# Kernel tuning notes

Hardware: AMD Instinct MI355X
Metric: run time of the kernel (lower is better)

Reference implementation:

```python
import jax, jax.numpy as jnp
import numpy as np

N = 512          # num_satellites
STATE_DIM = 6    # pos(3) + vel(3)
OBJ_DIM = 58
F = STATE_DIM + OBJ_DIM          # node feature dim = 64
HID = (128, 64, 32)
EDGE_IN = 2 * F + 1              # sender + receiver + distance
NODE_IN = F + HID[-1]            # node feats + aggregated messages


def _linear_init(key, d_in, d_out):
    kw, _ = jax.random.split(key)
    w = jax.random.normal(kw, (d_in, d_out), jnp.float32) / np.sqrt(d_in).astype(np.float32)
    b = jnp.zeros((d_out,), jnp.float32)
    return w, b


def setup_inputs() -> dict:
    key = jax.random.key(0)
    ks = jax.random.split(key, 12)
    ew0, eb0 = _linear_init(ks[0], EDGE_IN, HID[0])
    ew1, eb1 = _linear_init(ks[1], HID[0], HID[1])
    ew2, eb2 = _linear_init(ks[2], HID[1], HID[2])
    nw0, nb0 = _linear_init(ks[3], NODE_IN, HID[0])
    nw1, nb1 = _linear_init(ks[4], HID[0], HID[1])
    nw2, nb2 = _linear_init(ks[5], HID[1], HID[2])
    nwo, nbo = _linear_init(ks[6], HID[2], F)   # residual projection back to F
    rw, rb = _linear_init(ks[7], F, 3)          # control readout
    states = jax.random.normal(ks[8], (N, STATE_DIM), jnp.float32)
    objectives = jax.random.normal(ks[9], (OBJ_DIM,), jnp.float32)
    return dict(states=states, objectives=objectives,
                ew0=ew0, eb0=eb0, ew1=ew1, eb1=eb1, ew2=ew2, eb2=eb2,
                nw0=nw0, nb0=nb0, nw1=nw1, nb1=nb1, nw2=nw2, nb2=nb2,
                nwo=nwo, nbo=nbo, rw=rw, rb=rb,
                num_message_passing=3)


def _edge_index(n):
    ii, jj = np.meshgrid(np.arange(n), np.arange(n), indexing='ij')
    m = ii != jj
    return jnp.asarray(ii[m]), jnp.asarray(jj[m])  # sender i, receiver j; E = n*(n-1)


def reference(states, objectives, ew0, eb0, ew1, eb1, ew2, eb2,
              nw0, nb0, nw1, nb1, nw2, nb2, nwo, nbo, rw, rb,
              num_message_passing):
    n = states.shape[0]
    snd, rcv = _edge_index(n)
    # node features: state concat broadcast objectives -> [N, F]
    nf = jnp.concatenate(
        [states, jnp.broadcast_to(objectives, (n, objectives.shape[0]))], axis=-1)
    # distances from raw states (constant across iterations): [E, 1]
    rel = states[rcv, :3] - states[snd, :3]
    dist = jnp.linalg.norm(rel, axis=-1, keepdims=True)
    relu = jax.nn.relu
    for _ in range(num_message_passing):
        # edge MLP over all E edges: [E, 2F+1] -> [E, 32]
        x = jnp.concatenate([nf[snd], nf[rcv], dist], axis=-1)
        h = relu(x @ ew0 + eb0)
        h = relu(h @ ew1 + eb1)
        msg = relu(h @ ew2 + eb2)
        # sum-aggregate incoming messages at receiver j: [N, 32]
        agg = jax.ops.segment_sum(msg, rcv, num_segments=n)
        # node MLP + residual: [N, F+32] -> [N, F]
        y = jnp.concatenate([nf, agg], axis=-1)
        h = relu(y @ nw0 + nb0)
        h = relu(h @ nw1 + nb1)
        h = relu(h @ nw2 + nb2)
        nf = nf + h @ nwo + nbo
    # control readout: [N, 3]
    return nf @ rw + rb
```

## Files before the change

### kernel.cpp

```cpp
#include <hip/hip_runtime.h>
#include <math.h>

#define NSAT 512
#define FDIM 64
#define H0D  128
#define H1D  64
#define H2D  32
#define NGRP 8
#define SB   64

#define KP1 68

#define WS_NF    0
#define WS_PRES  (WS_NF   + NSAT * FDIM)
#define WS_PRER  (WS_PRES + NSAT * H0D)
#define WS_AGG   (WS_PRER + NSAT * H0D)
#define WS_WT    (WS_AGG  + NGRP * NSAT * H2D)

using short8_t = __attribute__((ext_vector_type(8))) short;
using short4_t = __attribute__((ext_vector_type(4))) short;
using floatx4  = __attribute__((ext_vector_type(4))) float;
using floatx16 = __attribute__((ext_vector_type(16))) float;

__device__ __forceinline__ void split_ru(float x, short& hi, short& lo) {
    unsigned u = __builtin_bit_cast(unsigned, x);
    unsigned hb = (u + 0x8000u) >> 16;
    hi = (short)hb;
    float r = x - __builtin_bit_cast(float, hb << 16);
    lo = (short)((__builtin_bit_cast(unsigned, r) + 0x8000u) >> 16);
}

__global__ void prep_weights_kernel(const float* __restrict__ ew1,
                                    const float* __restrict__ ew2,
                                    short* __restrict__ w1A_hi,
                                    short* __restrict__ w1A_lo,
                                    short* __restrict__ w2t_hi,
                                    short* __restrict__ w2t_lo) {
    int e = blockIdx.x * 256 + threadIdx.x;
    if (e < H1D * H0D) {
        int j  = e & 7;
        int l  = (e >> 3) & 63;
        int kk = (e >> 9) & 7;
        int mh = e >> 12;
        int m = mh * 32 + (l & 31);
        int k = (l >> 5) * 64 + kk * 8 + j;
        short hi, lo; split_ru(ew1[k * H1D + m], hi, lo);
        w1A_hi[e] = hi; w1A_lo[e] = lo;
    } else if (e < H1D * H0D + H2D * H1D) {
        int e2 = e - H1D * H0D;
        int c = e2 >> 6, k = e2 & 63;
        short hi, lo; split_ru(ew2[k * H2D + c], hi, lo);
        w2t_hi[e2] = hi; w2t_lo[e2] = lo;
    }
}

__device__ __forceinline__ void compute_pre(const float* __restrict__ nfl,
                                            const float* __restrict__ ew0,
                                            const float* __restrict__ eb0,
                                            int i, int t,
                                            float* __restrict__ preSA,
                                            float* __restrict__ preR) {
    if (t < H0D) {
        int k = t;
        float s0 = 0.f, s1 = 0.f, s2 = 0.f, s3 = 0.f;
        #pragma unroll
        for (int f = 0; f < FDIM; f += 4) {
            s0 = fmaf(nfl[f + 0], ew0[(f + 0) * H0D + k], s0);
            s1 = fmaf(nfl[f + 1], ew0[(f + 1) * H0D + k], s1);
            s2 = fmaf(nfl[f + 2], ew0[(f + 2) * H0D + k], s2);
            s3 = fmaf(nfl[f + 3], ew0[(f + 3) * H0D + k], s3);
        }
        int kk = (k >> 3) & 7, lhi = k >> 6, j = k & 7;
        preSA[((i >> 5) * 8 + kk) * 512 + (lhi * 32 + (i & 31)) * 8 + j] =
            (s0 + s1) + (s2 + s3);
    } else {
        int k = t - H0D;
        float s0 = eb0[k], s1 = 0.f, s2 = 0.f, s3 = 0.f;
        #pragma unroll
        for (int f = 0; f < FDIM; f += 4) {
            s0 = fmaf(nfl[f + 0], ew0[(FDIM + f + 0) * H0D + k], s0);
            s1 = fmaf(nfl[f + 1], ew0[(FDIM + f + 1) * H0D + k], s1);
            s2 = fmaf(nfl[f + 2], ew0[(FDIM + f + 2) * H0D + k], s2);
            s3 = fmaf(nfl[f + 3], ew0[(FDIM + f + 3) * H0D + k], s3);
        }
        preR[i * H0D + k] = (s0 + s1) + (s2 + s3);
    }
}

__global__ void init_node_kernel(const float* __restrict__ states,
                                 const float* __restrict__ objectives,
                                 const float* __restrict__ ew0,
                                 const float* __restrict__ eb0,
                                 float* __restrict__ nf,
                                 float* __restrict__ preSA,
                                 float* __restrict__ preR) {
    __shared__ float nfl[FDIM];
    int i = blockIdx.x, t = threadIdx.x;
    if (t < FDIM) {
        float v = (t < 6) ? states[i * 6 + t] : objectives[t - 6];
        nfl[t] = v;
        nf[i * FDIM + t] = v;
    }
    __syncthreads();
    compute_pre(nfl, ew0, eb0, i, t, preSA, preR);
}

__global__ __launch_bounds__(256, 4)
void edge_agg_kernel(const float* __restrict__ states,
                     const float* __restrict__ preSA,
                     const float* __restrict__ preR,
                     const float* __restrict__ ew0,
                     const float* __restrict__ eb1,
                     const float* __restrict__ eb2,
                     const short* __restrict__ w1A_hi,
                     const short* __restrict__ w1A_lo,
                     const short* __restrict__ w2t_hi,
                     const short* __restrict__ w2t_lo,
                     float* __restrict__ aggP) {
    __shared__ __align__(16) short h1_hi[SB * KP1];
    __shared__ __align__(16) short h1_lo[SB * KP1];
    __shared__ __align__(16) float preR_l[H0D];
    __shared__ __align__(16) float wd_l[H0D];
    __shared__ float d_l[SB];
    __shared__ __align__(16) float eb1_l[H1D];
    __shared__ float eb2_l[H2D];
    __shared__ __align__(16) float red_l[4 * H2D];

    int t = threadIdx.x, b = blockIdx.x;
    int j = b >> 3, g = b & 7;
    int w = t >> 6, lane = t & 63;
    int mhalf = w >> 1, shalf = w & 1;
    int lhi = lane >> 5, llo = lane & 31;

    if (t < H0D) preR_l[t] = preR[j * H0D + t];
    else         wd_l[t - H0D] = ew0[H0D * H0D + (t - H0D)];
    if (t < SB) {
        int s = g * SB + t;
        float dx = states[s * 6 + 0] - states[j * 6 + 0];
        float dy = states[s * 6 + 1] - states[j * 6 + 1];
        float dz = states[s * 6 + 2] - states[j * 6 + 2];
        d_l[t] = sqrtf(dx * dx + dy * dy + dz * dz);
    } else if (t < 128) {
        eb1_l[t - 64] = eb1[t - 64];
    } else if (t < 160) {
        eb2_l[t - 128] = eb2[t - 128];
    }
    __syncthreads();

    int G = g * 2 + shalf;
    float d = d_l[shalf * 32 + llo];
    const float* pS = preSA + (G * 8) * 512 + lane * 8;
    const short* pAh = w1A_hi + mhalf * 4096 + lane * 8;
    const short* pAl = w1A_lo + mhalf * 4096 + lane * 8;

    floatx16 acc1;
    #pragma unroll
    for (int r = 0; r < 16; ++r) acc1[r] = 0.f;

    #pragma unroll
    for (int kk = 0; kk < 8; ++kk) {
        float4 a0 = *(const float4*)(pS + kk * 512);
        float4 a1 = *(const float4*)(pS + kk * 512 + 4);
        int kb = lhi * 64 + kk * 8;
        float4 r0 = *(const float4*)&preR_l[kb];
        float4 r1 = *(const float4*)&preR_l[kb + 4];
        float4 q0 = *(const float4*)&wd_l[kb];
        float4 q1 = *(const float4*)&wd_l[kb + 4];
        float v[8];
        v[0] = fmaxf(a0.x + fmaf(d, q0.x, r0.x), 0.f);
        v[1] = fmaxf(a0.y + fmaf(d, q0.y, r0.y), 0.f);
        v[2] = fmaxf(a0.z + fmaf(d, q0.z, r0.z), 0.f);
        v[3] = fmaxf(a0.w + fmaf(d, q0.w, r0.w), 0.f);
        v[4] = fmaxf(a1.x + fmaf(d, q1.x, r1.x), 0.f);
        v[5] = fmaxf(a1.y + fmaf(d, q1.y, r1.y), 0.f);
        v[6] = fmaxf(a1.z + fmaf(d, q1.z, r1.z), 0.f);
        v[7] = fmaxf(a1.w + fmaf(d, q1.w, r1.w), 0.f);
        short8_t bh, bl;
        #pragma unroll
        for (int e = 0; e < 8; ++e) {
            short hi, lo; split_ru(v[e], hi, lo);
            bh[e] = hi; bl[e] = lo;
        }
        short8_t ah = *(const short8_t*)(pAh + kk * 512);
        short8_t al = *(const short8_t*)(pAl + kk * 512);
        acc1 = __builtin_amdgcn_mfma_f32_32x32x16_bf16(ah, bh, acc1, 0, 0, 0);
        acc1 = __builtin_amdgcn_mfma_f32_32x32x16_bf16(ah, bl, acc1, 0, 0, 0);
        acc1 = __builtin_amdgcn_mfma_f32_32x32x16_bf16(al, bh, acc1, 0, 0, 0);
    }

    {
        int s1 = shalf * 32 + llo;
        #pragma unroll
        for (int q = 0; q < 4; ++q) {
            int m0 = mhalf * 32 + q * 8 + lhi * 4;
            short4_t ph, pl; short hi, lo;
            #pragma unroll
            for (int r = 0; r < 4; ++r) {
                float v = fmaxf(acc1[q * 4 + r] + eb1_l[m0 + r], 0.f);
                split_ru(v, hi, lo);
                ph[r] = hi; pl[r] = lo;
            }
            *(short4_t*)&h1_hi[s1 * KP1 + m0] = ph;
            *(short4_t*)&h1_lo[s1 * KP1 + m0] = pl;
        }
    }
    __syncthreads();

    int lq = lane >> 4, l15 = lane & 15;
    int s2loc = w * 16 + l15;
    floatx4 acc2a, acc2b;
    #pragma unroll
    for (int r = 0; r < 4; ++r) { acc2a[r] = 0.f; acc2b[r] = 0.f; }
    int bo2 = s2loc * KP1 + lq * 8;
    const short* pA2h0 = w2t_hi + l15 * H1D + lq * 8;
    const short* pA2l0 = w2t_lo + l15 * H1D + lq * 8;
    const short* pA2h1 = w2t_hi + (16 + l15) * H1D + lq * 8;
    const short* pA2l1 = w2t_lo + (16 + l15) * H1D + lq * 8;
    #pragma unroll
    for (int kk = 0; kk < 2; ++kk) {
        short4_t b0 = *(const short4_t*)&h1_hi[bo2 + kk * 32];
        short4_t b1 = *(const short4_t*)&h1_hi[bo2 + kk * 32 + 4];
        short4_t c0 = *(const short4_t*)&h1_lo[bo2 + kk * 32];
        short4_t c1 = *(const short4_t*)&h1_lo[bo2 + kk * 32 + 4];
        short8_t bh = __builtin_shufflevector(b0, b1, 0, 1, 2, 3, 4, 5, 6, 7);
        short8_t bl = __builtin_shufflevector(c0, c1, 0, 1, 2, 3, 4, 5, 6, 7);
        short8_t a0h = *(const short8_t*)(pA2h0 + kk * 32);
        short8_t a0l = *(const short8_t*)(pA2l0 + kk * 32);
        short8_t a1h = *(const short8_t*)(pA2h1 + kk * 32);
        short8_t a1l = *(const short8_t*)(pA2l1 + kk * 32);
        acc2a = __builtin_amdgcn_mfma_f32_16x16x32_bf16(a0h, bh, acc2a, 0, 0, 0);
        acc2a = __builtin_amdgcn_mfma_f32_16x16x32_bf16(a0h, bl, acc2a, 0, 0, 0);
        acc2a = __builtin_amdgcn_mfma_f32_16x16x32_bf16(a0l, bh, acc2a, 0, 0, 0);
        acc2b = __builtin_amdgcn_mfma_f32_16x16x32_bf16(a1h, bh, acc2b, 0, 0, 0);
        acc2b = __builtin_amdgcn_mfma_f32_16x16x32_bf16(a1h, bl, acc2b, 0, 0, 0);
        acc2b = __builtin_amdgcn_mfma_f32_16x16x32_bf16(a1l, bh, acc2b, 0, 0, 0);
    }

    {
        int sg = g * SB + s2loc;
        bool self = (sg == j);
        float red[8];
        #pragma unroll
        for (int r = 0; r < 4; ++r) {
            float v = fmaxf(acc2a[r] + eb2_l[lq * 4 + r], 0.f);
            if (self) v = 0.f;
            v += __shfl_xor(v, 1, 64); v += __shfl_xor(v, 2, 64);
            v += __shfl_xor(v, 4, 64); v += __shfl_xor(v, 8, 64);
            red[r] = v;
        }
        #pragma unroll
        for (int r = 0; r < 4; ++r) {
            float v = fmaxf(acc2b[r] + eb2_l[16 + lq * 4 + r], 0.f);
            if (self) v = 0.f;
            v += __shfl_xor(v, 1, 64); v += __shfl_xor(v, 2, 64);
            v += __shfl_xor(v, 4, 64); v += __shfl_xor(v, 8, 64);
            red[4 + r] = v;
        }
        if (l15 == 0) {
            *(float4*)&red_l[w * H2D + lq * 4] =
                make_float4(red[0], red[1], red[2], red[3]);
            *(float4*)&red_l[w * H2D + 16 + lq * 4] =
                make_float4(red[4], red[5], red[6], red[7]);
        }
    }
    __syncthreads();
    if (t < H2D) {
        float s = red_l[t] + red_l[H2D + t] + red_l[2 * H2D + t] + red_l[3 * H2D + t];
        aggP[(g * NSAT + j) * H2D + t] = s;
    }
}

__global__ __launch_bounds__(256)
void node_fused_kernel(const float* __restrict__ aggP,
                       const float* __restrict__ nw0, const float* __restrict__ nb0,
                       const float* __restrict__ nw1, const float* __restrict__ nb1,
                       const float* __restrict__ nw2, const float* __restrict__ nb2,
                       const float* __restrict__ nwo, const float* __restrict__ nbo,
                       const float* __restrict__ ew0, const float* __restrict__ eb0,
                       const float* __restrict__ rw,  const float* __restrict__ rb,
                       float* __restrict__ nf,
                       float* __restrict__ preSA,
                       float* __restrict__ preR,
                       float* __restrict__ out,
                       int final_iter) {
    __shared__ float y[96];
    __shared__ float hA[H0D];
    __shared__ float hB[H1D];
    __shared__ float hC[H2D];
    __shared__ float nfl[FDIM];
    int i = blockIdx.x, t = threadIdx.x;
    if (t < FDIM) y[t] = nf[i * FDIM + t];
    else if (t < 96) {
        int c = t - FDIM;
        float s = 0.f;
        #pragma unroll
        for (int g = 0; g < NGRP; ++g) s += aggP[(g * NSAT + i) * H2D + c];
        y[t] = s;
    }
    __syncthreads();
    if (t < H0D) {
        float s0 = nb0[t], s1 = 0.f, s2 = 0.f, s3 = 0.f;
        #pragma unroll
        for (int f = 0; f < 96; f += 4) {
            s0 = fmaf(y[f + 0], nw0[(f + 0) * H0D + t], s0);
            s1 = fmaf(y[f + 1], nw0[(f + 1) * H0D + t], s1);
            s2 = fmaf(y[f + 2], nw0[(f + 2) * H0D + t], s2);
            s3 = fmaf(y[f + 3], nw0[(f + 3) * H0D + t], s3);
        }
        hA[t] = fmaxf((s0 + s1) + (s2 + s3), 0.f);
    }
    __syncthreads();
    if (t < H1D) {
        float s0 = nb1[t], s1 = 0.f, s2 = 0.f, s3 = 0.f;
        #pragma unroll
        for (int k = 0; k < H0D; k += 4) {
            s0 = fmaf(hA[k + 0], nw1[(k + 0) * H1D + t], s0);
            s1 = fmaf(hA[k + 1], nw1[(k + 1) * H1D + t], s1);
            s2 = fmaf(hA[k + 2], nw1[(k + 2) * H1D + t], s2);
            s3 = fmaf(hA[k + 3], nw1[(k + 3) * H1D + t], s3);
        }
        hB[t] = fmaxf((s0 + s1) + (s2 + s3), 0.f);
    }
    __syncthreads();
    if (t < H2D) {
        float s0 = nb2[t], s1 = 0.f, s2 = 0.f, s3 = 0.f;
        #pragma unroll
        for (int m = 0; m < H1D; m += 4) {
            s0 = fmaf(hB[m + 0], nw2[(m + 0) * H2D + t], s0);
            s1 = fmaf(hB[m + 1], nw2[(m + 1) * H2D + t], s1);
            s2 = fmaf(hB[m + 2], nw2[(m + 2) * H2D + t], s2);
            s3 = fmaf(hB[m + 3], nw2[(m + 3) * H2D + t], s3);
        }
        hC[t] = fmaxf((s0 + s1) + (s2 + s3), 0.f);
    }
    __syncthreads();
    if (t < FDIM) {
        float s = nbo[t];
        #pragma unroll
        for (int c = 0; c < H2D; ++c) s = fmaf(hC[c], nwo[c * FDIM + t], s);
        float v = y[t] + s;
        nfl[t] = v;
        if (!final_iter) nf[i * FDIM + t] = v;
    }
    __syncthreads();
    if (final_iter) {
        if (t < 3) {
            float s0 = rb[t], s1 = 0.f, s2 = 0.f, s3 = 0.f;
            #pragma unroll
            for (int f = 0; f < FDIM; f += 4) {
                s0 = fmaf(nfl[f + 0], rw[(f + 0) * 3 + t], s0);
                s1 = fmaf(nfl[f + 1], rw[(f + 1) * 3 + t], s1);
                s2 = fmaf(nfl[f + 2], rw[(f + 2) * 3 + t], s2);
                s3 = fmaf(nfl[f + 3], rw[(f + 3) * 3 + t], s3);
            }
            out[i * 3 + t] = (s0 + s1) + (s2 + s3);
        }
    } else {
        compute_pre(nfl, ew0, eb0, i, t, preSA, preR);
    }
}

extern "C" void kernel_launch(void* const* d_in, const int* in_sizes, int n_in,
                              void* d_out, int out_size, void* d_ws, size_t ws_size,
                              hipStream_t stream) {
    const float* states     = (const float*)d_in[0];
    const float* objectives = (const float*)d_in[1];
    const float* ew0 = (const float*)d_in[2];
    const float* eb0 = (const float*)d_in[3];
    const float* ew1 = (const float*)d_in[4];
    const float* eb1 = (const float*)d_in[5];
    const float* ew2 = (const float*)d_in[6];
    const float* eb2 = (const float*)d_in[7];
    const float* nw0 = (const float*)d_in[8];
    const float* nb0 = (const float*)d_in[9];
    const float* nw1 = (const float*)d_in[10];
    const float* nb1 = (const float*)d_in[11];
    const float* nw2 = (const float*)d_in[12];
    const float* nb2 = (const float*)d_in[13];
    const float* nwo = (const float*)d_in[14];
    const float* nbo = (const float*)d_in[15];
    const float* rw  = (const float*)d_in[16];
    const float* rb  = (const float*)d_in[17];
    float* out = (float*)d_out;
    float* ws  = (float*)d_ws;

    float* nf    = ws + WS_NF;
    float* preSA = ws + WS_PRES;
    float* preR  = ws + WS_PRER;
    float* aggP  = ws + WS_AGG;
    short* w1A_hi = (short*)(ws + WS_WT);
    short* w1A_lo = w1A_hi + H1D * H0D;
    short* w2t_hi = w1A_lo + H1D * H0D;
    short* w2t_lo = w2t_hi + H2D * H1D;

    prep_weights_kernel<<<40, 256, 0, stream>>>(ew1, ew2, w1A_hi, w1A_lo,
                                                w2t_hi, w2t_lo);
    init_node_kernel<<<NSAT, 256, 0, stream>>>(states, objectives, ew0, eb0,
                                               nf, preSA, preR);
    for (int it = 0; it < 3; ++it) {
        edge_agg_kernel<<<NGRP * NSAT, 256, 0, stream>>>(states, preSA, preR,
                                                         ew0, eb1, eb2,
                                                         w1A_hi, w1A_lo,
                                                         w2t_hi, w2t_lo, aggP);
        node_fused_kernel<<<NSAT, 256, 0, stream>>>(aggP, nw0, nb0, nw1, nb1,
                                                    nw2, nb2, nwo, nbo,
                                                    ew0, eb0, rw, rb,
                                                    nf, preSA, preR, out,
                                                    (it == 2) ? 1 : 0);
    }
}
```

Before: 212.6 us.

## Fuse edge aggregation and node MLP into one per-receiver kernel per iteration

Merges the edge-MLP/aggregation kernel and the node-MLP kernel into a single iter_kernel where each block owns one receiver and loops over all 512 senders in four 128-sender chunks. Partial aggregates stay in registers and shared memory instead of being written to a global aggP buffer. preSA/preR are double-buffered across iterations to avoid read/write races, weight prep and init are merged into one setup launch, and the hi/lo bf16 split uses packed perm instructions. The cost is that the grid shrinks from 4096 blocks to 512 with a serial loop per block, which lowers parallelism and occupancy on the edge phase.

```diff
diff --git a/kernel.cpp b/kernel.cpp
--- a/kernel.cpp
+++ b/kernel.cpp
@@ -6,19 +6,20 @@
 #define H0D  128
 #define H1D  64
 #define H2D  32
-#define NGRP 8
-#define SB   64
-
-#define KP1 68
+#define SBG  128
+#define KP1  68
 
 #define WS_NF    0
-#define WS_PRES  (WS_NF   + NSAT * FDIM)
-#define WS_PRER  (WS_PRES + NSAT * H0D)
-#define WS_AGG   (WS_PRER + NSAT * H0D)
-#define WS_WT    (WS_AGG  + NGRP * NSAT * H2D)
+#define WS_PRES0 (WS_NF    + NSAT * FDIM)
+#define WS_PRER0 (WS_PRES0 + NSAT * H0D)
+#define WS_PRES1 (WS_PRER0 + NSAT * H0D)
+#define WS_PRER1 (WS_PRES1 + NSAT * H0D)
+#define WS_WT    (WS_PRER1 + NSAT * H0D)
 
 using short8_t = __attribute__((ext_vector_type(8))) short;
 using short4_t = __attribute__((ext_vector_type(4))) short;
+using int4_t   = __attribute__((ext_vector_type(4))) int;
+using int2_t   = __attribute__((ext_vector_type(2))) int;
 using floatx4  = __attribute__((ext_vector_type(4))) float;
 using floatx16 = __attribute__((ext_vector_type(16))) float;
 
@@ -30,28 +31,44 @@
     lo = (short)((__builtin_bit_cast(unsigned, r) + 0x8000u) >> 16);
 }
 
-__global__ void prep_weights_kernel(const float* __restrict__ ew1,
-                                    const float* __restrict__ ew2,
-                                    short* __restrict__ w1A_hi,
-                                    short* __restrict__ w1A_lo,
-                                    short* __restrict__ w2t_hi,
-                                    short* __restrict__ w2t_lo) {
-    int e = blockIdx.x * 256 + threadIdx.x;
-    if (e < H1D * H0D) {
-        int j  = e & 7;
-        int l  = (e >> 3) & 63;
-        int kk = (e >> 9) & 7;
-        int mh = e >> 12;
-        int m = mh * 32 + (l & 31);
-        int k = (l >> 5) * 64 + kk * 8 + j;
-        short hi, lo; split_ru(ew1[k * H1D + m], hi, lo);
-        w1A_hi[e] = hi; w1A_lo[e] = lo;
-    } else if (e < H1D * H0D + H2D * H1D) {
-        int e2 = e - H1D * H0D;
-        int c = e2 >> 6, k = e2 & 63;
-        short hi, lo; split_ru(ew2[k * H2D + c], hi, lo);
-        w2t_hi[e2] = hi; w2t_lo[e2] = lo;
-    }
+__device__ __forceinline__ void split8_pk(const float* __restrict__ v,
+                                          short8_t& bh, short8_t& bl) {
+    unsigned t[8]; unsigned ru[8];
+    #pragma unroll
+    for (int e = 0; e < 8; ++e) {
+        unsigned u = __builtin_bit_cast(unsigned, v[e]);
+        t[e] = u + 0x8000u;
+        float r = v[e] - __builtin_bit_cast(float, t[e] & 0xffff0000u);
+        ru[e] = __builtin_bit_cast(unsigned, r);
+    }
+    int4_t hv, lv;
+    #pragma unroll
+    for (int p = 0; p < 4; ++p) {
+        hv[p] = (int)__builtin_amdgcn_perm(t[2*p+1],  t[2*p],  0x07060302u);
+        lv[p] = (int)__builtin_amdgcn_perm(ru[2*p+1], ru[2*p], 0x07060302u);
+    }
+    bh = __builtin_bit_cast(short8_t, hv);
+    bl = __builtin_bit_cast(short8_t, lv);
+}
+
+__device__ __forceinline__ void split4_pk(const float* __restrict__ v,
+                                          short4_t& h, short4_t& l) {
+    unsigned t[4]; unsigned ru[4];
+    #pragma unroll
+    for (int e = 0; e < 4; ++e) {
+        unsigned u = __builtin_bit_cast(unsigned, v[e]);
+        t[e] = u + 0x8000u;
+        float r = v[e] - __builtin_bit_cast(float, t[e] & 0xffff0000u);
+        ru[e] = __builtin_bit_cast(unsigned, r);
+    }
+    int2_t hv, lv;
+    #pragma unroll
+    for (int p = 0; p < 2; ++p) {
+        hv[p] = (int)__builtin_amdgcn_perm(t[2*p+1],  t[2*p],  0x07060302u);
+        lv[p] = (int)__builtin_amdgcn_perm(ru[2*p+1], ru[2*p], 0x07060302u);
+    }
+    h = __builtin_bit_cast(short4_t, hv);
+    l = __builtin_bit_cast(short4_t, lv);
 }
 
 __device__ __forceinline__ void compute_pre(const float* __restrict__ nfl,
@@ -87,260 +104,294 @@
     }
 }
 
-__global__ void init_node_kernel(const float* __restrict__ states,
-                                 const float* __restrict__ objectives,
-                                 const float* __restrict__ ew0,
-                                 const float* __restrict__ eb0,
-                                 float* __restrict__ nf,
-                                 float* __restrict__ preSA,
-                                 float* __restrict__ preR) {
+__global__ void setup_kernel(const float* __restrict__ states,
+                             const float* __restrict__ objectives,
+                             const float* __restrict__ ew0,
+                             const float* __restrict__ eb0,
+                             const float* __restrict__ ew1,
+                             const float* __restrict__ ew2,
+                             float* __restrict__ nf,
+                             float* __restrict__ preSA,
+                             float* __restrict__ preR,
+                             short* __restrict__ w1A_hi,
+                             short* __restrict__ w1A_lo,
+                             short* __restrict__ w2t_hi,
+                             short* __restrict__ w2t_lo) {
     __shared__ float nfl[FDIM];
-    int i = blockIdx.x, t = threadIdx.x;
-    if (t < FDIM) {
-        float v = (t < 6) ? states[i * 6 + t] : objectives[t - 6];
-        nfl[t] = v;
-        nf[i * FDIM + t] = v;
-    }
-    __syncthreads();
-    compute_pre(nfl, ew0, eb0, i, t, preSA, preR);
-}
-
-__global__ __launch_bounds__(256, 4)
-void edge_agg_kernel(const float* __restrict__ states,
-                     const float* __restrict__ preSA,
-                     const float* __restrict__ preR,
-                     const float* __restrict__ ew0,
-                     const float* __restrict__ eb1,
-                     const float* __restrict__ eb2,
-                     const short* __restrict__ w1A_hi,
-                     const short* __restrict__ w1A_lo,
-                     const short* __restrict__ w2t_hi,
-                     const short* __restrict__ w2t_lo,
-                     float* __restrict__ aggP) {
-    __shared__ __align__(16) short h1_hi[SB * KP1];
-    __shared__ __align__(16) short h1_lo[SB * KP1];
+    int b = blockIdx.x, t = threadIdx.x;
+    if (b < NSAT) {
+        if (t < FDIM) {
+            float v = (t < 6) ? states[b * 6 + t] : objectives[t - 6];
+            nfl[t] = v;
+            nf[b * FDIM + t] = v;
+        }
+        __syncthreads();
+        compute_pre(nfl, ew0, eb0, b, t, preSA, preR);
+    } else {
+        int e = (b - NSAT) * 256 + t;
+        if (e < H1D * H0D) {
+            int j  = e & 7;
+            int l  = (e >> 3) & 63;
+            int kk = (e >> 9) & 7;
+            int mh = e >> 12;
+            int m = mh * 32 + (l & 31);
+            int k = (l >> 5) * 64 + kk * 8 + j;
+            short hi, lo; split_ru(ew1[k * H1D + m], hi, lo);
+            w1A_hi[e] = hi; w1A_lo[e] = lo;
+        } else if (e < H1D * H0D + H2D * H1D) {
+            int e2 = e - H1D * H0D;
+            int c = e2 >> 6, k = e2 & 63;
+            short hi, lo; split_ru(ew2[k * H2D + c], hi, lo);
+            w2t_hi[e2] = hi; w2t_lo[e2] = lo;
+        }
+    }
+}
+
+__global__ __launch_bounds__(256)
+void iter_kernel(const float* __restrict__ states,
+                 const float* __restrict__ preSA_in,
+                 const float* __restrict__ preR_in,
+                 const float* __restrict__ ew0,
+                 const float* __restrict__ eb0,
+                 const float* __restrict__ eb1,
+                 const float* __restrict__ eb2,
+                 const short* __restrict__ w1A_hi,
+                 const short* __restrict__ w1A_lo,
+                 const short* __restrict__ w2t_hi,
+                 const short* __restrict__ w2t_lo,
+                 const float* __restrict__ nw0, const float* __restrict__ nb0,
+                 const float* __restrict__ nw1, const float* __restrict__ nb1,
+                 const float* __restrict__ nw2, const float* __restrict__ nb2,
+                 const float* __restrict__ nwo, const float* __restrict__ nbo,
+                 const float* __restrict__ rw,  const float* __restrict__ rb,
+                 float* __restrict__ nf,
+                 float* __restrict__ preSA_out,
+                 float* __restrict__ preR_out,
+                 float* __restrict__ out,
+                 int final_iter) {
+    __shared__ __align__(16) short h1_hi[SBG * KP1];
+    __shared__ __align__(16) short h1_lo[SBG * KP1];
     __shared__ __align__(16) float preR_l[H0D];
     __shared__ __align__(16) float wd_l[H0D];
-    __shared__ float d_l[SB];
+    __shared__ float d_l[NSAT];
     __shared__ __align__(16) float eb1_l[H1D];
     __shared__ float eb2_l[H2D];
     __shared__ __align__(16) float red_l[4 * H2D];
-
-    int t = threadIdx.x, b = blockIdx.x;
-    int j = b >> 3, g = b & 7;
+    __shared__ float yv[96];
+    __shared__ float hA_l[H0D];
+    __shared__ float hB_l[H1D];
+    __shared__ float hC_l[H2D];
+    __shared__ float nfl_l[FDIM];
+
+    int t = threadIdx.x, j = blockIdx.x;
     int w = t >> 6, lane = t & 63;
-    int mhalf = w >> 1, shalf = w & 1;
     int lhi = lane >> 5, llo = lane & 31;
 
-    if (t < H0D) preR_l[t] = preR[j * H0D + t];
+    if (t < H0D) preR_l[t] = preR_in[j * H0D + t];
     else         wd_l[t - H0D] = ew0[H0D * H0D + (t - H0D)];
-    if (t < SB) {
-        int s = g * SB + t;
-        float dx = states[s * 6 + 0] - states[j * 6 + 0];
-        float dy = states[s * 6 + 1] - states[j * 6 + 1];
-        float dz = states[s * 6 + 2] - states[j * 6 + 2];
-        d_l[t] = sqrtf(dx * dx + dy * dy + dz * dz);
-    } else if (t < 128) {
-        eb1_l[t - 64] = eb1[t - 64];
-    } else if (t < 160) {
-        eb2_l[t - 128] = eb2[t - 128];
-    }
-    __syncthreads();
-
-    int G = g * 2 + shalf;
-    float d = d_l[shalf * 32 + llo];
-    const float* pS = preSA + (G * 8) * 512 + lane * 8;
-    const short* pAh = w1A_hi + mhalf * 4096 + lane * 8;
-    const short* pAl = w1A_lo + mhalf * 4096 + lane * 8;
-
-    floatx16 acc1;
-    #pragma unroll
-    for (int r = 0; r < 16; ++r) acc1[r] = 0.f;
-
-    #pragma unroll
-    for (int kk = 0; kk < 8; ++kk) {
-        float4 a0 = *(const float4*)(pS + kk * 512);
-        float4 a1 = *(const float4*)(pS + kk * 512 + 4);
-        int kb = lhi * 64 + kk * 8;
-        float4 r0 = *(const float4*)&preR_l[kb];
-        float4 r1 = *(const float4*)&preR_l[kb + 4];
-        float4 q0 = *(const float4*)&wd_l[kb];
-        float4 q1 = *(const float4*)&wd_l[kb + 4];
-        float v[8];
-        v[0] = fmaxf(a0.x + fmaf(d, q0.x, r0.x), 0.f);
-        v[1] = fmaxf(a0.y + fmaf(d, q0.y, r0.y), 0.f);
-        v[2] = fmaxf(a0.z + fmaf(d, q0.z, r0.z), 0.f);
-        v[3] = fmaxf(a0.w + fmaf(d, q0.w, r0.w), 0.f);
-        v[4] = fmaxf(a1.x + fmaf(d, q1.x, r1.x), 0.f);
-        v[5] = fmaxf(a1.y + fmaf(d, q1.y, r1.y), 0.f);
-        v[6] = fmaxf(a1.z + fmaf(d, q1.z, r1.z), 0.f);
-        v[7] = fmaxf(a1.w + fmaf(d, q1.w, r1.w), 0.f);
-        short8_t bh, bl;
-        #pragma unroll
-        for (int e = 0; e < 8; ++e) {
-            short hi, lo; split_ru(v[e], hi, lo);
-            bh[e] = hi; bl[e] = lo;
-        }
-        short8_t ah = *(const short8_t*)(pAh + kk * 512);
-        short8_t al = *(const short8_t*)(pAl + kk * 512);
-        acc1 = __builtin_amdgcn_mfma_f32_32x32x16_bf16(ah, bh, acc1, 0, 0, 0);
-        acc1 = __builtin_amdgcn_mfma_f32_32x32x16_bf16(ah, bl, acc1, 0, 0, 0);
-        acc1 = __builtin_amdgcn_mfma_f32_32x32x16_bf16(al, bh, acc1, 0, 0, 0);
-    }
-
-    {
-        int s1 = shalf * 32 + llo;
-        #pragma unroll
-        for (int q = 0; q < 4; ++q) {
-            int m0 = mhalf * 32 + q * 8 + lhi * 4;
-            short4_t ph, pl; short hi, lo;
+    if (t < 64)       { eb1_l[t] = eb1[t]; yv[t] = nf[j * FDIM + t]; }
+    else if (t < 96)  { eb2_l[t - 64] = eb2[t - 64]; }
+    float pjx = states[j * 6 + 0], pjy = states[j * 6 + 1], pjz = states[j * 6 + 2];
+    for (int s = t; s < NSAT; s += 256) {
+        float dx = states[s * 6 + 0] - pjx;
+        float dy = states[s * 6 + 1] - pjy;
+        float dz = states[s * 6 + 2] - pjz;
+        d_l[s] = sqrtf(dx * dx + dy * dy + dz * dz);
+    }
+    __syncthreads();
+
+    float aggAcc = 0.f;
+
+    for (int G4 = 0; G4 < 4; ++G4) {
+        const float* pS = preSA_in + (size_t)((G4 * 4 + w) * 8) * 512 + lane * 8;
+        const short* pAh0 = w1A_hi + lane * 8;
+        const short* pAl0 = w1A_lo + lane * 8;
+        float d = d_l[G4 * SBG + w * 32 + llo];
+
+        floatx16 accA, accB;
+        #pragma unroll
+        for (int r = 0; r < 16; ++r) { accA[r] = 0.f; accB[r] = 0.f; }
+
+        #pragma unroll
+        for (int kk = 0; kk < 8; ++kk) {
+            float4 a0 = *(const float4*)(pS + kk * 512);
+            float4 a1 = *(const float4*)(pS + kk * 512 + 4);
+            int kb = lhi * 64 + kk * 8;
+            float4 r0 = *(const float4*)&preR_l[kb];
+            float4 r1 = *(const float4*)&preR_l[kb + 4];
+            float4 q0 = *(const float4*)&wd_l[kb];
+            float4 q1 = *(const float4*)&wd_l[kb + 4];
+            float v[8];
+            v[0] = fmaxf(a0.x + fmaf(d, q0.x, r0.x), 0.f);
+            v[1] = fmaxf(a0.y + fmaf(d, q0.y, r0.y), 0.f);
+            v[2] = fmaxf(a0.z + fmaf(d, q0.z, r0.z), 0.f);
+            v[3] = fmaxf(a0.w + fmaf(d, q0.w, r0.w), 0.f);
+            v[4] = fmaxf(a1.x + fmaf(d, q1.x, r1.x), 0.f);
+            v[5] = fmaxf(a1.y + fmaf(d, q1.y, r1.y), 0.f);
+            v[6] = fmaxf(a1.z + fmaf(d, q1.z, r1.z), 0.f);
+            v[7] = fmaxf(a1.w + fmaf(d, q1.w, r1.w), 0.f);
+            short8_t bh, bl;
+            split8_pk(v, bh, bl);
+            short8_t ah0 = *(const short8_t*)(pAh0 + kk * 512);
+            short8_t al0 = *(const short8_t*)(pAl0 + kk * 512);
+            short8_t ah1 = *(const short8_t*)(pAh0 + 4096 + kk * 512);
+            short8_t al1 = *(const short8_t*)(pAl0 + 4096 + kk * 512);
+            accA = __builtin_amdgcn_mfma_f32_32x32x16_bf16(ah0, bh, accA, 0, 0, 0);
+            accA = __builtin_amdgcn_mfma_f32_32x32x16_bf16(ah0, bl, accA, 0, 0, 0);
+            accA = __builtin_amdgcn_mfma_f32_32x32x16_bf16(al0, bh, accA, 0, 0, 0);
+            accB = __builtin_amdgcn_mfma_f32_32x32x16_bf16(ah1, bh, accB, 0, 0, 0);
+            accB = __builtin_amdgcn_mfma_f32_32x32x16_bf16(ah1, bl, accB, 0, 0, 0);
+            accB = __builtin_amdgcn_mfma_f32_32x32x16_bf16(al1, bh, accB, 0, 0, 0);
+        }
+
+        {
+            int s1 = w * 32 + llo;
+            #pragma unroll
+            for (int mh = 0; mh < 2; ++mh) {
+                #pragma unroll
+                for (int q = 0; q < 4; ++q) {
+                    int m0 = mh * 32 + q * 8 + lhi * 4;
+                    float vv[4];
+                    #pragma unroll
+                    for (int r = 0; r < 4; ++r) {
+                        float c = mh ? accB[q * 4 + r] : accA[q * 4 + r];
+                        vv[r] = fmaxf(c + eb1_l[m0 + r], 0.f);
+                    }
+                    short4_t ph, pl;
+                    split4_pk(vv, ph, pl);
+                    *(short4_t*)&h1_hi[s1 * KP1 + m0] = ph;
+                    *(short4_t*)&h1_lo[s1 * KP1 + m0] = pl;
+                }
+            }
+        }
+        __syncthreads();
+
+        int lq = lane >> 4, l15 = lane & 15;
+        int sA = w * 32 + l15, sB = sA + 16;
+        floatx4 aA0, aA1, aB0, aB1;
+        #pragma unroll
+        for (int r = 0; r < 4; ++r) { aA0[r]=0.f; aA1[r]=0.f; aB0[r]=0.f; aB1[r]=0.f; }
+        const short* pA2h0 = w2t_hi + l15 * H1D + lq * 8;
+        const short* pA2l0 = w2t_lo + l15 * H1D + lq * 8;
+        const short* pA2h1 = w2t_hi + (16 + l15) * H1D + lq * 8;
+        const short* pA2l1 = w2t_lo + (16 + l15) * H1D + lq * 8;
+        int boA = sA * KP1 + lq * 8, boB = sB * KP1 + lq * 8;
+        #pragma unroll
+        for (int kk = 0; kk < 2; ++kk) {
+            short4_t b0, b1, c0, c1;
+            b0 = *(const short4_t*)&h1_hi[boA + kk * 32];
+            b1 = *(const short4_t*)&h1_hi[boA + kk * 32 + 4];
+            c0 = *(const short4_t*)&h1_lo[boA + kk * 32];
+            c1 = *(const short4_t*)&h1_lo[boA + kk * 32 + 4];
+            short8_t bhA = __builtin_shufflevector(b0, b1, 0,1,2,3,4,5,6,7);
+            short8_t blA = __builtin_shufflevector(c0, c1, 0,1,2,3,4,5,6,7);
+            b0 = *(const short4_t*)&h1_hi[boB + kk * 32];
+            b1 = *(const short4_t*)&h1_hi[boB + kk * 32 + 4];
+            c0 = *(const short4_t*)&h1_lo[boB + kk * 32];
+            c1 = *(const short4_t*)&h1_lo[boB + kk * 32 + 4];
+            short8_t bhB = __builtin_shufflevector(b0, b1, 0,1,2,3,4,5,6,7);
+            short8_t blB = __builtin_shufflevector(c0, c1, 0,1,2,3,4,5,6,7);
+            short8_t a0h = *(const short8_t*)(pA2h0 + kk * 32);
+            short8_t a0l = *(const short8_t*)(pA2l0 + kk * 32);
+            short8_t a1h = *(const short8_t*)(pA2h1 + kk * 32);
+            short8_t a1l = *(const short8_t*)(pA2l1 + kk * 32);
+            aA0 = __builtin_amdgcn_mfma_f32_16x16x32_bf16(a0h, bhA, aA0, 0, 0, 0);
+            aA0 = __builtin_amdgcn_mfma_f32_16x16x32_bf16(a0h, blA, aA0, 0, 0, 0);
+            aA0 = __builtin_amdgcn_mfma_f32_16x16x32_bf16(a0l, bhA, aA0, 0, 0, 0);
+            aA1 = __builtin_amdgcn_mfma_f32_16x16x32_bf16(a1h, bhA, aA1, 0, 0, 0);
+            aA1 = __builtin_amdgcn_mfma_f32_16x16x32_bf16(a1h, blA, aA1, 0, 0, 0);
+            aA1 = __builtin_amdgcn_mfma_f32_16x16x32_bf16(a1l, bhA, aA1, 0, 0, 0);
+            aB0 = __builtin_amdgcn_mfma_f32_16x16x32_bf16(a0h, bhB, aB0, 0, 0, 0);
+            aB0 = __builtin_amdgcn_mfma_f32_16x16x32_bf16(a0h, blB, aB0, 0, 0, 0);
+            aB0 = __builtin_amdgcn_mfma_f32_16x16x32_bf16(a0l, bhB, aB0, 0, 0, 0);
+            aB1 = __builtin_amdgcn_mfma_f32_16x16x32_bf16(a1h, bhB, aB1, 0, 0, 0);
+            aB1 = __builtin_amdgcn_mfma_f32_16x16x32_bf16(a1h, blB, aB1, 0, 0, 0);
+            aB1 = __builtin_amdgcn_mfma_f32_16x16x32_bf16(a1l, bhB, aB1, 0, 0, 0);
+        }
+
+        {
+            bool selfA = (G4 * SBG + sA == j);
+            bool selfB = (G4 * SBG + sB == j);
+            float red[8];
             #pragma unroll
             for (int r = 0; r < 4; ++r) {
-                float v = fmaxf(acc1[q * 4 + r] + eb1_l[m0 + r], 0.f);
-                split_ru(v, hi, lo);
-                ph[r] = hi; pl[r] = lo;
+                float vA = fmaxf(aA0[r] + eb2_l[lq * 4 + r], 0.f);
+                float vB = fmaxf(aB0[r] + eb2_l[lq * 4 + r], 0.f);
+                if (selfA) vA = 0.f;
+                if (selfB) vB = 0.f;
+                float v = vA + vB;
+                v += __shfl_xor(v, 1, 64); v += __shfl_xor(v, 2, 64);
+                v += __shfl_xor(v, 4, 64); v += __shfl_xor(v, 8, 64);
+                red[r] = v;
             }
-            *(short4_t*)&h1_hi[s1 * KP1 + m0] = ph;
-            *(short4_t*)&h1_lo[s1 * KP1 + m0] = pl;
-        }
-    }
-    __syncthreads();
-
-    int lq = lane >> 4, l15 = lane & 15;
-    int s2loc = w * 16 + l15;
-    floatx4 acc2a, acc2b;
-    #pragma unroll
-    for (int r = 0; r < 4; ++r) { acc2a[r] = 0.f; acc2b[r] = 0.f; }
-    int bo2 = s2loc * KP1 + lq * 8;
-    const short* pA2h0 = w2t_hi + l15 * H1D + lq * 8;
-    const short* pA2l0 = w2t_lo + l15 * H1D + lq * 8;
-    const short* pA2h1 = w2t_hi + (16 + l15) * H1D + lq * 8;
-    const short* pA2l1 = w2t_lo + (16 + l15) * H1D + lq * 8;
-    #pragma unroll
-    for (int kk = 0; kk < 2; ++kk) {
-        short4_t b0 = *(const short4_t*)&h1_hi[bo2 + kk * 32];
-        short4_t b1 = *(const short4_t*)&h1_hi[bo2 + kk * 32 + 4];
-        short4_t c0 = *(const short4_t*)&h1_lo[bo2 + kk * 32];
-        short4_t c1 = *(const short4_t*)&h1_lo[bo2 + kk * 32 + 4];
-        short8_t bh = __builtin_shufflevector(b0, b1, 0, 1, 2, 3, 4, 5, 6, 7);
-        short8_t bl = __builtin_shufflevector(c0, c1, 0, 1, 2, 3, 4, 5, 6, 7);
-        short8_t a0h = *(const short8_t*)(pA2h0 + kk * 32);
-        short8_t a0l = *(const short8_t*)(pA2l0 + kk * 32);
-        short8_t a1h = *(const short8_t*)(pA2h1 + kk * 32);
-        short8_t a1l = *(const short8_t*)(pA2l1 + kk * 32);
-        acc2a = __builtin_amdgcn_mfma_f32_16x16x32_bf16(a0h, bh, acc2a, 0, 0, 0);
-        acc2a = __builtin_amdgcn_mfma_f32_16x16x32_bf16(a0h, bl, acc2a, 0, 0, 0);
-        acc2a = __builtin_amdgcn_mfma_f32_16x16x32_bf16(a0l, bh, acc2a, 0, 0, 0);
-        acc2b = __builtin_amdgcn_mfma_f32_16x16x32_bf16(a1h, bh, acc2b, 0, 0, 0);
-        acc2b = __builtin_amdgcn_mfma_f32_16x16x32_bf16(a1h, bl, acc2b, 0, 0, 0);
-        acc2b = __builtin_amdgcn_mfma_f32_16x16x32_bf16(a1l, bh, acc2b, 0, 0, 0);
-    }
-
-    {
-        int sg = g * SB + s2loc;
-        bool self = (sg == j);
-        float red[8];
-        #pragma unroll
-        for (int r = 0; r < 4; ++r) {
-            float v = fmaxf(acc2a[r] + eb2_l[lq * 4 + r], 0.f);
-            if (self) v = 0.f;
-            v += __shfl_xor(v, 1, 64); v += __shfl_xor(v, 2, 64);
-            v += __shfl_xor(v, 4, 64); v += __shfl_xor(v, 8, 64);
-            red[r] = v;
-        }
-        #pragma unroll
-        for (int r = 0; r < 4; ++r) {
-            float v = fmaxf(acc2b[r] + eb2_l[16 + lq * 4 + r], 0.f);
-            if (self) v = 0.f;
-            v += __shfl_xor(v, 1, 64); v += __shfl_xor(v, 2, 64);
-            v += __shfl_xor(v, 4, 64); v += __shfl_xor(v, 8, 64);
-            red[4 + r] = v;
-        }
-        if (l15 == 0) {
-            *(float4*)&red_l[w * H2D + lq * 4] =
-                make_float4(red[0], red[1], red[2], red[3]);
-            *(float4*)&red_l[w * H2D + 16 + lq * 4] =
-                make_float4(red[4], red[5], red[6], red[7]);
-        }
-    }
-    __syncthreads();
-    if (t < H2D) {
-        float s = red_l[t] + red_l[H2D + t] + red_l[2 * H2D + t] + red_l[3 * H2D + t];
-        aggP[(g * NSAT + j) * H2D + t] = s;
-    }
-}
-
-__global__ __launch_bounds__(256)
-void node_fused_kernel(const float* __restrict__ aggP,
-                       const float* __restrict__ nw0, const float* __restrict__ nb0,
-                       const float* __restrict__ nw1, const float* __restrict__ nb1,
-                       const float* __restrict__ nw2, const float* __restrict__ nb2,
-                       const float* __restrict__ nwo, const float* __restrict__ nbo,
-                       const float* __restrict__ ew0, const float* __restrict__ eb0,
-                       const float* __restrict__ rw,  const float* __restrict__ rb,
-                       float* __restrict__ nf,
-                       float* __restrict__ preSA,
-                       float* __restrict__ preR,
-                       float* __restrict__ out,
-                       int final_iter) {
-    __shared__ float y[96];
-    __shared__ float hA[H0D];
-    __shared__ float hB[H1D];
-    __shared__ float hC[H2D];
-    __shared__ float nfl[FDIM];
-    int i = blockIdx.x, t = threadIdx.x;
-    if (t < FDIM) y[t] = nf[i * FDIM + t];
-    else if (t < 96) {
-        int c = t - FDIM;
-        float s = 0.f;
-        #pragma unroll
-        for (int g = 0; g < NGRP; ++g) s += aggP[(g * NSAT + i) * H2D + c];
-        y[t] = s;
-    }
+            #pragma unroll
+            for (int r = 0; r < 4; ++r) {
+                float vA = fmaxf(aA1[r] + eb2_l[16 + lq * 4 + r], 0.f);
+                float vB = fmaxf(aB1[r] + eb2_l[16 + lq * 4 + r], 0.f);
+                if (selfA) vA = 0.f;
+                if (selfB) vB = 0.f;
+                float v = vA + vB;
+                v += __shfl_xor(v, 1, 64); v += __shfl_xor(v, 2, 64);
+                v += __shfl_xor(v, 4, 64); v += __shfl_xor(v, 8, 64);
+                red[4 + r] = v;
+            }
+            if (l15 == 0) {
+                *(float4*)&red_l[w * H2D + lq * 4] =
+                    make_float4(red[0], red[1], red[2], red[3]);
+                *(float4*)&red_l[w * H2D + 16 + lq * 4] =
+                    make_float4(red[4], red[5], red[6], red[7]);
+            }
+        }
+        __syncthreads();
+        if (t < H2D)
+            aggAcc += red_l[t] + red_l[H2D + t] + red_l[2*H2D + t] + red_l[3*H2D + t];
+    }
+
+    if (t < H2D) yv[64 + t] = aggAcc;
     __syncthreads();
     if (t < H0D) {
         float s0 = nb0[t], s1 = 0.f, s2 = 0.f, s3 = 0.f;
         #pragma unroll
         for (int f = 0; f < 96; f += 4) {
-            s0 = fmaf(y[f + 0], nw0[(f + 0) * H0D + t], s0);
-            s1 = fmaf(y[f + 1], nw0[(f + 1) * H0D + t], s1);
-            s2 = fmaf(y[f + 2], nw0[(f + 2) * H0D + t], s2);
-            s3 = fmaf(y[f + 3], nw0[(f + 3) * H0D + t], s3);
-        }
-        hA[t] = fmaxf((s0 + s1) + (s2 + s3), 0.f);
+            s0 = fmaf(yv[f + 0], nw0[(f + 0) * H0D + t], s0);
+            s1 = fmaf(yv[f + 1], nw0[(f + 1) * H0D + t], s1);
+            s2 = fmaf(yv[f + 2], nw0[(f + 2) * H0D + t], s2);
+            s3 = fmaf(yv[f + 3], nw0[(f + 3) * H0D + t], s3);
+        }
+        hA_l[t] = fmaxf((s0 + s1) + (s2 + s3), 0.f);
     }
     __syncthreads();
     if (t < H1D) {
         float s0 = nb1[t], s1 = 0.f, s2 = 0.f, s3 = 0.f;
         #pragma unroll
         for (int k = 0; k < H0D; k += 4) {
-            s0 = fmaf(hA[k + 0], nw1[(k + 0) * H1D + t], s0);
-            s1 = fmaf(hA[k + 1], nw1[(k + 1) * H1D + t], s1);
-            s2 = fmaf(hA[k + 2], nw1[(k + 2) * H1D + t], s2);
-            s3 = fmaf(hA[k + 3], nw1[(k + 3) * H1D + t], s3);
-        }
-        hB[t] = fmaxf((s0 + s1) + (s2 + s3), 0.f);
+            s0 = fmaf(hA_l[k + 0], nw1[(k + 0) * H1D + t], s0);
+            s1 = fmaf(hA_l[k + 1], nw1[(k + 1) * H1D + t], s1);
+            s2 = fmaf(hA_l[k + 2], nw1[(k + 2) * H1D + t], s2);
+            s3 = fmaf(hA_l[k + 3], nw1[(k + 3) * H1D + t], s3);
+        }
+        hB_l[t] = fmaxf((s0 + s1) + (s2 + s3), 0.f);
     }
     __syncthreads();
     if (t < H2D) {
         float s0 = nb2[t], s1 = 0.f, s2 = 0.f, s3 = 0.f;
         #pragma unroll
         for (int m = 0; m < H1D; m += 4) {
-            s0 = fmaf(hB[m + 0], nw2[(m + 0) * H2D + t], s0);
-            s1 = fmaf(hB[m + 1], nw2[(m + 1) * H2D + t], s1);
-            s2 = fmaf(hB[m + 2], nw2[(m + 2) * H2D + t], s2);
-            s3 = fmaf(hB[m + 3], nw2[(m + 3) * H2D + t], s3);
-        }
-        hC[t] = fmaxf((s0 + s1) + (s2 + s3), 0.f);
+            s0 = fmaf(hB_l[m + 0], nw2[(m + 0) * H2D + t], s0);
+            s1 = fmaf(hB_l[m + 1], nw2[(m + 1) * H2D + t], s1);
+            s2 = fmaf(hB_l[m + 2], nw2[(m + 2) * H2D + t], s2);
+            s3 = fmaf(hB_l[m + 3], nw2[(m + 3) * H2D + t], s3);
+        }
+        hC_l[t] = fmaxf((s0 + s1) + (s2 + s3), 0.f);
     }
     __syncthreads();
     if (t < FDIM) {
         float s = nbo[t];
         #pragma unroll
-        for (int c = 0; c < H2D; ++c) s = fmaf(hC[c], nwo[c * FDIM + t], s);
-        float v = y[t] + s;
-        nfl[t] = v;
-        if (!final_iter) nf[i * FDIM + t] = v;
+        for (int c = 0; c < H2D; ++c) s = fmaf(hC_l[c], nwo[c * FDIM + t], s);
+        float v = yv[t] + s;
+        nfl_l[t] = v;
+        if (!final_iter) nf[j * FDIM + t] = v;
     }
     __syncthreads();
     if (final_iter) {
@@ -348,15 +399,15 @@
             float s0 = rb[t], s1 = 0.f, s2 = 0.f, s3 = 0.f;
             #pragma unroll
             for (int f = 0; f < FDIM; f += 4) {
-                s0 = fmaf(nfl[f + 0], rw[(f + 0) * 3 + t], s0);
-                s1 = fmaf(nfl[f + 1], rw[(f + 1) * 3 + t], s1);
-                s2 = fmaf(nfl[f + 2], rw[(f + 2) * 3 + t], s2);
-                s3 = fmaf(nfl[f + 3], rw[(f + 3) * 3 + t], s3);
+                s0 = fmaf(nfl_l[f + 0], rw[(f + 0) * 3 + t], s0);
+                s1 = fmaf(nfl_l[f + 1], rw[(f + 1) * 3 + t], s1);
+                s2 = fmaf(nfl_l[f + 2], rw[(f + 2) * 3 + t], s2);
+                s3 = fmaf(nfl_l[f + 3], rw[(f + 3) * 3 + t], s3);
             }
-            out[i * 3 + t] = (s0 + s1) + (s2 + s3);
+            out[j * 3 + t] = (s0 + s1) + (s2 + s3);
         }
     } else {
-        compute_pre(nfl, ew0, eb0, i, t, preSA, preR);
+        compute_pre(nfl_l, ew0, eb0, j, t, preSA_out, preR_out);
     }
 }
 
@@ -384,28 +435,29 @@
     float* out = (float*)d_out;
     float* ws  = (float*)d_ws;
 
-    float* nf    = ws + WS_NF;
-    float* preSA = ws + WS_PRES;
-    float* preR  = ws + WS_PRER;
-    float* aggP  = ws + WS_AGG;
+    float* nf     = ws + WS_NF;
+    float* preSA0 = ws + WS_PRES0;
+    float* preR0  = ws + WS_PRER0;
+    float* preSA1 = ws + WS_PRES1;
+    float* preR1  = ws + WS_PRER1;
     short* w1A_hi = (short*)(ws + WS_WT);
     short* w1A_lo = w1A_hi + H1D * H0D;
     short* w2t_hi = w1A_lo + H1D * H0D;
     short* w2t_lo = w2t_hi + H2D * H1D;
 
-    prep_weights_kernel<<<40, 256, 0, stream>>>(ew1, ew2, w1A_hi, w1A_lo,
-                                                w2t_hi, w2t_lo);
-    init_node_kernel<<<NSAT, 256, 0, stream>>>(states, objectives, ew0, eb0,
-                                               nf, preSA, preR);
-    for (int it = 0; it < 3; ++it) {
-        edge_agg_kernel<<<NGRP * NSAT, 256, 0, stream>>>(states, preSA, preR,
-                                                         ew0, eb1, eb2,
-                                                         w1A_hi, w1A_lo,
-                                                         w2t_hi, w2t_lo, aggP);
-        node_fused_kernel<<<NSAT, 256, 0, stream>>>(aggP, nw0, nb0, nw1, nb1,
-                                                    nw2, nb2, nwo, nbo,
-                                                    ew0, eb0, rw, rb,
-                                                    nf, preSA, preR, out,
-                                                    (it == 2) ? 1 : 0);
-    }
-}
+    setup_kernel<<<NSAT + 40, 256, 0, stream>>>(states, objectives, ew0, eb0,
+                                                ew1, ew2, nf, preSA0, preR0,
+                                                w1A_hi, w1A_lo, w2t_hi, w2t_lo);
+    iter_kernel<<<NSAT, 256, 0, stream>>>(states, preSA0, preR0, ew0, eb0, eb1,
+                                          eb2, w1A_hi, w1A_lo, w2t_hi, w2t_lo,
+                                          nw0, nb0, nw1, nb1, nw2, nb2, nwo, nbo,
+                                          rw, rb, nf, preSA1, preR1, out, 0);
+    iter_kernel<<<NSAT, 256, 0, stream>>>(states, preSA1, preR1, ew0, eb0, eb1,
+                                          eb2, w1A_hi, w1A_lo, w2t_hi, w2t_lo,
+                                          nw0, nb0, nw1, nb1, nw2, nb2, nwo, nbo,
+                                          rw, rb, nf, preSA0, preR0, out, 0);
+    iter_kernel<<<NSAT, 256, 0, stream>>>(states, preSA0, preR0, ew0, eb0, eb1,
+                                          eb2, w1A_hi, w1A_lo, w2t_hi, w2t_lo,
+                                          nw0, nb0, nw1, nb1, nw2, nb2, nwo, nbo,
+                                          rw, rb, nf, preSA1, preR1, out, 1);
+}
```

Measured after the change: 222.9 us. 4.8% more time.
